# Optimization experiments

Hardware: AMD Instinct MI355X
Metric: run time of the kernel (lower is better)

## Reference

```python
import jax, jax.numpy as jnp
import numpy as np

N = 50000      # nodes
E = 800000     # edges (avg degree 16)
D = 128        # node_dim
H = 3          # total_hops
NE = 16        # num edge types
LN_EPS = 1e-3  # keras LayerNormalization default


def setup_inputs() -> dict:
    key = jax.random.key(0)
    ks = jax.random.split(key, 8)
    scale = 1.0 / np.sqrt(D)
    return {
        "x": jax.random.normal(ks[0], (N, D), jnp.float32),
        "src": jax.random.randint(ks[1], (E,), 0, N, jnp.int32),
        "dest": jax.random.randint(ks[2], (E,), 0, N, jnp.int32),
        "classes": jax.random.randint(ks[3], (E,), 0, NE, jnp.int32),
        "W_src": jax.random.normal(ks[4], (H, D, D), jnp.float32) * scale,
        "b_src": jnp.zeros((H, D), jnp.float32),
        "W_dest": jax.random.normal(ks[5], (H, D, D), jnp.float32) * scale,
        "b_dest": jnp.zeros((H, D), jnp.float32),
        "edge_emb": jax.random.normal(ks[6], (H, NE, D), jnp.float32) * 0.02,
        "ln_gamma": jnp.ones((H, D), jnp.float32),
        "ln_beta": jnp.zeros((H, D), jnp.float32),
    }


def _hop(x, src, dest, classes, Ws, bs, Wd, bd, ee, g, b):
    # dense transforms on nodes [N,D], then gather to edges [E,D]
    s = x @ Ws + bs
    t = x @ Wd + bd
    msgs = jax.nn.relu(s[src] + t[dest] + ee[classes])  # [E,D]
    # unsorted_segment_mean: zero for empty segments (TF semantics)
    summ = jax.ops.segment_sum(msgs, dest, num_segments=N)                    # [N,D]
    cnt = jax.ops.segment_sum(jnp.ones((E, 1), x.dtype), dest, num_segments=N)
    mean = jnp.where(cnt > 0, summ / jnp.maximum(cnt, 1.0), 0.0)
    y = mean + x  # residual add
    mu = jnp.mean(y, axis=-1, keepdims=True)
    var = jnp.mean(jnp.square(y - mu), axis=-1, keepdims=True)
    return g * (y - mu) * jax.lax.rsqrt(var + LN_EPS) + b


def reference(x, src, dest, classes, W_src, b_src, W_dest, b_dest, edge_emb, ln_gamma, ln_beta):
    for i in range(H):
        x = _hop(x, src, dest, classes, W_src[i], b_src[i], W_dest[i], b_dest[i],
                 edge_emb[i], ln_gamma[i], ln_beta[i])
    return x
```

## Files before the change

### kernel.cpp

```cpp
#include <hip/hip_runtime.h>

#define D 128
#define NE 16
#define HOPS 3
#define CAP 96
#define CPAD 32

typedef __attribute__((ext_vector_type(8))) __bf16 bf16x8;
typedef __attribute__((ext_vector_type(4))) __bf16 bf16x4;
typedef __attribute__((ext_vector_type(4))) float f32x4;

#define PK_MASK 0x07FFFFFFu
#define PK_SHIFT 27

__global__ __launch_bounds__(256) void prep_kernel(
    const int* __restrict__ src, const int* __restrict__ dest,
    const int* __restrict__ classes, int* __restrict__ cnt,
    unsigned int* __restrict__ s_pk, int E, int FB,
    const float* __restrict__ Wsrc, const float* __restrict__ Wdst,
    __bf16* __restrict__ WTs, __bf16* __restrict__ WTd, int WB,
    const float* __restrict__ x, __bf16* __restrict__ xb, int n4, int CB) {
  int b = blockIdx.x;
  int tid = threadIdx.x;
  if (b < FB) {
    int e = b * 256 + tid;
    if (e < E) {
      int d = dest[e];
      int p = atomicAdd(&cnt[(size_t)d * CPAD], 1);
      if (p < CAP)
        s_pk[(size_t)d * CAP + p] = (unsigned int)src[e] | ((unsigned int)classes[e] << PK_SHIFT);
    }
  } else if (b < FB + WB) {
    int gid = (b - FB) * 256 + tid;
    int h = gid >> 14;
    int rem = gid & 16383;
    int k = rem >> 7, nn = rem & 127;
    size_t o = (size_t)h * 16384 + nn * 128 + k;
    WTs[o] = (__bf16)Wsrc[gid];
    WTd[o] = (__bf16)Wdst[gid];
  } else {
    int i = (b - FB - WB) * 256 + tid;
    if (i < n4) {
      f32x4 v = ((const f32x4*)x)[i];
      bf16x4 o;
      o[0] = (__bf16)v[0]; o[1] = (__bf16)v[1]; o[2] = (__bf16)v[2]; o[3] = (__bf16)v[3];
      ((bf16x4*)xb)[i] = o;
    }
  }
}

__global__ __launch_bounds__(256) void gemm_dual(const __bf16* __restrict__ xb,
    const __bf16* __restrict__ WTs, const __bf16* __restrict__ WTd,
    const float* __restrict__ bs, const float* __restrict__ bd,
    __bf16* __restrict__ s_b, __bf16* __restrict__ t_b, int n) {
  int w = threadIdx.x >> 6, l = threadIdx.x & 63;
  int l16 = l & 15, q = l >> 4;
  bf16x8 a[2][4];
  #pragma unroll
  for (int rt = 0; rt < 2; ++rt) {
    int rowA = blockIdx.x * 128 + (w + rt * 4) * 16 + l16;
    int rsafe = rowA < n ? rowA : 0;
    #pragma unroll
    for (int ks = 0; ks < 4; ++ks)
      a[rt][ks] = *(const bf16x8*)&xb[(size_t)rsafe * D + ks * 32 + q * 8];
  }
  f32x4 accS[2][8], accT[2][8];
  #pragma unroll
  for (int rt = 0; rt < 2; ++rt)
    #pragma unroll
    for (int n0 = 0; n0 < 8; ++n0) {
      accS[rt][n0] = (f32x4)0.f;
      accT[rt][n0] = (f32x4)0.f;
    }
  #pragma unroll
  for (int n0 = 0; n0 < 8; ++n0) {
    const __bf16* ps = &WTs[(size_t)(n0 * 16 + l16) * D + q * 8];
    const __bf16* pt = &WTd[(size_t)(n0 * 16 + l16) * D + q * 8];
    #pragma unroll
    for (int ks = 0; ks < 4; ++ks) {
      bf16x8 bfs = *(const bf16x8*)(ps + ks * 32);
      bf16x8 bft = *(const bf16x8*)(pt + ks * 32);
      #pragma unroll
      for (int rt = 0; rt < 2; ++rt) {
        accS[rt][n0] = __builtin_amdgcn_mfma_f32_16x16x32_bf16(a[rt][ks], bfs, accS[rt][n0], 0, 0, 0);
        accT[rt][n0] = __builtin_amdgcn_mfma_f32_16x16x32_bf16(a[rt][ks], bft, accT[rt][n0], 0, 0, 0);
      }
    }
  }
  #pragma unroll
  for (int rt = 0; rt < 2; ++rt) {
    int rowD = blockIdx.x * 128 + (w + rt * 4) * 16 + q * 4;
    #pragma unroll
    for (int n0 = 0; n0 < 8; ++n0) {
      int col = n0 * 16 + l16;
      float bS = bs[col], bT = bd[col];
      #pragma unroll
      for (int r = 0; r < 4; ++r) {
        int row = rowD + r;
        if (row < n) {
          s_b[(size_t)row * D + col] = (__bf16)(accS[rt][n0][r] + bS);
          t_b[(size_t)row * D + col] = (__bf16)(accT[rt][n0][r] + bT);
        }
      }
    }
  }
}

__global__ __launch_bounds__(256) void aggregate_kernel(
    const __bf16* __restrict__ s_b, const __bf16* __restrict__ t_b,
    const float* __restrict__ xin,
    const int* __restrict__ cnt_arr,
    const unsigned int* __restrict__ s_pk,
    const float* __restrict__ ee, const float* __restrict__ gamma,
    const float* __restrict__ beta, float* __restrict__ xout,
    __bf16* __restrict__ xb_out, int write_xb, int n) {
  __shared__ float ee_s[NE * D];
  for (int i = threadIdx.x; i < NE * D; i += 256) ee_s[i] = ee[i];
  __syncthreads();
  int wave = threadIdx.x >> 6;
  int lane = threadIdx.x & 63;
  int node = blockIdx.x * 4 + wave;
  if (node >= n) return;
  int quarter = lane >> 4;
  int l16 = lane & 15;
  int d0 = l16 * 8;
  size_t nbase = (size_t)node * D;
  bf16x8 tvb = *(const bf16x8*)&t_b[nbase + d0];
  float tv[8];
  #pragma unroll
  for (int j = 0; j < 8; ++j) tv[j] = (float)tvb[j];
  f32x4 xlo = *(const f32x4*)&xin[nbase + d0];
  f32x4 xhi = *(const f32x4*)&xin[nbase + d0 + 4];
  int cn = cnt_arr[(size_t)node * CPAD];
  if (cn > CAP) cn = CAP;
  int beg = node * CAP;
  int end = beg + cn;
  float acc[8] = {0.f, 0.f, 0.f, 0.f, 0.f, 0.f, 0.f, 0.f};
  int e = beg + quarter;
  for (; e + 4 < end; e += 8) {
    unsigned int v0 = s_pk[e];
    unsigned int v1 = s_pk[e + 4];
    bf16x8 sv0 = *(const bf16x8*)&s_b[(size_t)(v0 & PK_MASK) * D + d0];
    bf16x8 sv1 = *(const bf16x8*)&s_b[(size_t)(v1 & PK_MASK) * D + d0];
    const float* ep0 = &ee_s[(v0 >> PK_SHIFT) * D + d0];
    const float* ep1 = &ee_s[(v1 >> PK_SHIFT) * D + d0];
    f32x4 e0a = *(const f32x4*)ep0, e0b = *(const f32x4*)(ep0 + 4);
    f32x4 e1a = *(const f32x4*)ep1, e1b = *(const f32x4*)(ep1 + 4);
    #pragma unroll
    for (int j = 0; j < 8; ++j) {
      float u0 = (float)sv0[j] + tv[j] + (j < 4 ? e0a[j] : e0b[j - 4]);
      float u1 = (float)sv1[j] + tv[j] + (j < 4 ? e1a[j] : e1b[j - 4]);
      acc[j] += fmaxf(u0, 0.f) + fmaxf(u1, 0.f);
    }
  }
  if (e < end) {
    unsigned int v0 = s_pk[e];
    bf16x8 sv0 = *(const bf16x8*)&s_b[(size_t)(v0 & PK_MASK) * D + d0];
    const float* ep0 = &ee_s[(v0 >> PK_SHIFT) * D + d0];
    f32x4 e0a = *(const f32x4*)ep0, e0b = *(const f32x4*)(ep0 + 4);
    #pragma unroll
    for (int j = 0; j < 8; ++j) {
      float u0 = (float)sv0[j] + tv[j] + (j < 4 ? e0a[j] : e0b[j - 4]);
      acc[j] += fmaxf(u0, 0.f);
    }
  }
  #pragma unroll
  for (int j = 0; j < 8; ++j) {
    acc[j] += __shfl_xor(acc[j], 32);
    acc[j] += __shfl_xor(acc[j], 16);
  }
  float invc = cn > 0 ? 1.f / (float)cn : 0.f;
  float y[8];
  #pragma unroll
  for (int j = 0; j < 8; ++j)
    y[j] = acc[j] * invc + (j < 4 ? xlo[j] : xhi[j - 4]);
  float ssum = 0.f;
  #pragma unroll
  for (int j = 0; j < 8; ++j) ssum += y[j];
  #pragma unroll
  for (int off = 8; off > 0; off >>= 1) ssum += __shfl_xor(ssum, off);
  float mu = ssum * (1.f / (float)D);
  float dv[8], vs = 0.f;
  #pragma unroll
  for (int j = 0; j < 8; ++j) { dv[j] = y[j] - mu; vs += dv[j] * dv[j]; }
  #pragma unroll
  for (int off = 8; off > 0; off >>= 1) vs += __shfl_xor(vs, off);
  float inv = rsqrtf(vs * (1.f / (float)D) + 1e-3f);
  if (quarter == 0) {
    f32x4 g0 = *(const f32x4*)&gamma[d0];
    f32x4 g1 = *(const f32x4*)&gamma[d0 + 4];
    f32x4 b0 = *(const f32x4*)&beta[d0];
    f32x4 b1 = *(const f32x4*)&beta[d0 + 4];
    float o[8];
    #pragma unroll
    for (int j = 0; j < 8; ++j)
      o[j] = (j < 4 ? g0[j] : g1[j - 4]) * dv[j] * inv + (j < 4 ? b0[j] : b1[j - 4]);
    f32x4 o0, o1;
    #pragma unroll
    for (int j = 0; j < 4; ++j) { o0[j] = o[j]; o1[j] = o[j + 4]; }
    *(f32x4*)&xout[nbase + d0] = o0;
    *(f32x4*)&xout[nbase + d0 + 4] = o1;
    if (write_xb) {
      bf16x8 ob;
      #pragma unroll
      for (int j = 0; j < 8; ++j) ob[j] = (__bf16)o[j];
      *(bf16x8*)&xb_out[nbase + d0] = ob;
    }
  }
}

extern "C" void kernel_launch(void* const* d_in, const int* in_sizes, int n_in,
                              void* d_out, int out_size, void* d_ws, size_t ws_size,
                              hipStream_t stream) {
  const float* x0     = (const float*)d_in[0];
  const int*   src    = (const int*)d_in[1];
  const int*   dest   = (const int*)d_in[2];
  const int*   cls    = (const int*)d_in[3];
  const float* W_src  = (const float*)d_in[4];
  const float* b_src  = (const float*)d_in[5];
  const float* W_dest = (const float*)d_in[6];
  const float* b_dest = (const float*)d_in[7];
  const float* ee     = (const float*)d_in[8];
  const float* ln_g   = (const float*)d_in[9];
  const float* ln_b   = (const float*)d_in[10];
  float* out = (float*)d_out;

  const int N = in_sizes[0] / D;
  const int E = in_sizes[1];

  char* p = (char*)d_ws;
  __bf16* s_b = (__bf16*)p;   p += (size_t)N * D * sizeof(__bf16);
  __bf16* t_b = (__bf16*)p;   p += (size_t)N * D * sizeof(__bf16);
  __bf16* xb  = (__bf16*)p;   p += (size_t)N * D * sizeof(__bf16);
  __bf16* WTs = (__bf16*)p;   p += (size_t)HOPS * D * D * sizeof(__bf16);
  __bf16* WTd = (__bf16*)p;   p += (size_t)HOPS * D * D * sizeof(__bf16);
  int* cntb   = (int*)p;      p += (size_t)N * CPAD * sizeof(int);
  unsigned int* s_pk = (unsigned int*)p; p += (size_t)N * CAP * sizeof(unsigned int);

  hipMemsetAsync(cntb, 0, (size_t)N * CPAD * sizeof(int), stream);

  const int FB = (E + 255) / 256;
  const int WB = (HOPS * D * D) / 256;
  const int n4 = N * D / 4;
  const int CB = (n4 + 255) / 256;
  prep_kernel<<<FB + WB + CB, 256, 0, stream>>>(
      src, dest, cls, cntb, s_pk, E, FB,
      W_src, W_dest, WTs, WTd, WB,
      x0, xb, n4, CB);

  const float* xin = x0;
  for (int h = 0; h < HOPS; ++h) {
    gemm_dual<<<(N + 127) / 128, 256, 0, stream>>>(
        xb, WTs + (size_t)h * D * D, WTd + (size_t)h * D * D,
        b_src + (size_t)h * D, b_dest + (size_t)h * D, s_b, t_b, N);
    aggregate_kernel<<<(N + 3) / 4, 256, 0, stream>>>(
        s_b, t_b, xin, cntb, s_pk,
        ee + (size_t)h * NE * D, ln_g + (size_t)h * D, ln_b + (size_t)h * D,
        out, xb, (h < HOPS - 1) ? 1 : 0, N);
    xin = out;
  }
}
```

Measured before the change: 291.5 us.

## Split per-node edge buckets into four sub-buckets with separate atomic counters

The bucketing step now spreads each node's incoming edges over four sub-buckets, one counter per sub-bucket placed on its own cache-line offset, chosen by edge index. This is meant to cut atomic contention on the per-node counter. The aggregation kernel gives each wave quarter its own sub-bucket and unrolls the gather loop four deep to keep more loads in flight. Load balance across quarters now depends on the edge distribution, and each sub-bucket caps at 24 entries, so a node whose edges crowd one sub-bucket can drop edges that the old 96-entry single bucket would have kept.

New measurement: 337.4 us. 15.8% more time.

```diff
diff --git a/kernel.cpp b/kernel.cpp
--- a/kernel.cpp
+++ b/kernel.cpp
@@ -3,7 +3,9 @@
 #define D 128
 #define NE 16
 #define HOPS 3
-#define CAP 96
+#define NSUB 4
+#define SCAP 24
+#define CAP (NSUB * SCAP)
 #define CPAD 32
 
 typedef __attribute__((ext_vector_type(8))) __bf16 bf16x8;
@@ -26,9 +28,11 @@
     int e = b * 256 + tid;
     if (e < E) {
       int d = dest[e];
-      int p = atomicAdd(&cnt[(size_t)d * CPAD], 1);
-      if (p < CAP)
-        s_pk[(size_t)d * CAP + p] = (unsigned int)src[e] | ((unsigned int)classes[e] << PK_SHIFT);
+      int sub = e & (NSUB - 1);
+      int p = atomicAdd(&cnt[(size_t)d * CPAD + sub * 8], 1);
+      if (p < SCAP)
+        s_pk[(size_t)d * CAP + sub * SCAP + p] =
+            (unsigned int)src[e] | ((unsigned int)classes[e] << PK_SHIFT);
     }
   } else if (b < FB + WB) {
     int gid = (b - FB) * 256 + tid;
@@ -131,45 +135,59 @@
   for (int j = 0; j < 8; ++j) tv[j] = (float)tvb[j];
   f32x4 xlo = *(const f32x4*)&xin[nbase + d0];
   f32x4 xhi = *(const f32x4*)&xin[nbase + d0 + 4];
-  int cn = cnt_arr[(size_t)node * CPAD];
-  if (cn > CAP) cn = CAP;
-  int beg = node * CAP;
-  int end = beg + cn;
+
+  int cq = cnt_arr[(size_t)node * CPAD + quarter * 8];
+  if (cq > SCAP) cq = SCAP;
+  int base = node * CAP + quarter * SCAP;
   float acc[8] = {0.f, 0.f, 0.f, 0.f, 0.f, 0.f, 0.f, 0.f};
-  int e = beg + quarter;
-  for (; e + 4 < end; e += 8) {
-    unsigned int v0 = s_pk[e];
-    unsigned int v1 = s_pk[e + 4];
-    bf16x8 sv0 = *(const bf16x8*)&s_b[(size_t)(v0 & PK_MASK) * D + d0];
-    bf16x8 sv1 = *(const bf16x8*)&s_b[(size_t)(v1 & PK_MASK) * D + d0];
-    const float* ep0 = &ee_s[(v0 >> PK_SHIFT) * D + d0];
-    const float* ep1 = &ee_s[(v1 >> PK_SHIFT) * D + d0];
-    f32x4 e0a = *(const f32x4*)ep0, e0b = *(const f32x4*)(ep0 + 4);
-    f32x4 e1a = *(const f32x4*)ep1, e1b = *(const f32x4*)(ep1 + 4);
-    #pragma unroll
-    for (int j = 0; j < 8; ++j) {
-      float u0 = (float)sv0[j] + tv[j] + (j < 4 ? e0a[j] : e0b[j - 4]);
-      float u1 = (float)sv1[j] + tv[j] + (j < 4 ? e1a[j] : e1b[j - 4]);
-      acc[j] += fmaxf(u0, 0.f) + fmaxf(u1, 0.f);
-    }
-  }
-  if (e < end) {
-    unsigned int v0 = s_pk[e];
-    bf16x8 sv0 = *(const bf16x8*)&s_b[(size_t)(v0 & PK_MASK) * D + d0];
-    const float* ep0 = &ee_s[(v0 >> PK_SHIFT) * D + d0];
-    f32x4 e0a = *(const f32x4*)ep0, e0b = *(const f32x4*)(ep0 + 4);
-    #pragma unroll
-    for (int j = 0; j < 8; ++j) {
-      float u0 = (float)sv0[j] + tv[j] + (j < 4 ? e0a[j] : e0b[j - 4]);
-      acc[j] += fmaxf(u0, 0.f);
-    }
-  }
+
+#define EDGE_ACC(V, SV)                                                        \
+  {                                                                            \
+    const float* ep = &ee_s[((V) >> PK_SHIFT) * D + d0];                       \
+    f32x4 ea = *(const f32x4*)ep, eb = *(const f32x4*)(ep + 4);                \
+    _Pragma("unroll")                                                          \
+    for (int j = 0; j < 8; ++j) {                                              \
+      float u = (float)(SV)[j] + tv[j] + (j < 4 ? ea[j] : eb[j - 4]);          \
+      acc[j] += fmaxf(u, 0.f);                                                 \
+    }                                                                          \
+  }
+
+  int i = 0;
+  for (; i + 3 < cq; i += 4) {
+    unsigned int v0 = s_pk[base + i];
+    unsigned int v1 = s_pk[base + i + 1];
+    unsigned int v2 = s_pk[base + i + 2];
+    unsigned int v3 = s_pk[base + i + 3];
+    bf16x8 s0 = *(const bf16x8*)&s_b[(size_t)(v0 & PK_MASK) * D + d0];
+    bf16x8 s1 = *(const bf16x8*)&s_b[(size_t)(v1 & PK_MASK) * D + d0];
+    bf16x8 s2 = *(const bf16x8*)&s_b[(size_t)(v2 & PK_MASK) * D + d0];
+    bf16x8 s3 = *(const bf16x8*)&s_b[(size_t)(v3 & PK_MASK) * D + d0];
+    EDGE_ACC(v0, s0); EDGE_ACC(v1, s1); EDGE_ACC(v2, s2); EDGE_ACC(v3, s3);
+  }
+  if (i + 1 < cq) {
+    unsigned int v0 = s_pk[base + i];
+    unsigned int v1 = s_pk[base + i + 1];
+    bf16x8 s0 = *(const bf16x8*)&s_b[(size_t)(v0 & PK_MASK) * D + d0];
+    bf16x8 s1 = *(const bf16x8*)&s_b[(size_t)(v1 & PK_MASK) * D + d0];
+    EDGE_ACC(v0, s0); EDGE_ACC(v1, s1);
+    i += 2;
+  }
+  if (i < cq) {
+    unsigned int v0 = s_pk[base + i];
+    bf16x8 s0 = *(const bf16x8*)&s_b[(size_t)(v0 & PK_MASK) * D + d0];
+    EDGE_ACC(v0, s0);
+  }
+#undef EDGE_ACC
+
+  int tot = cq;
+  tot += __shfl_xor(tot, 32);
+  tot += __shfl_xor(tot, 16);
   #pragma unroll
   for (int j = 0; j < 8; ++j) {
     acc[j] += __shfl_xor(acc[j], 32);
     acc[j] += __shfl_xor(acc[j], 16);
   }
-  float invc = cn > 0 ? 1.f / (float)cn : 0.f;
+  float invc = tot > 0 ? 1.f / (float)tot : 0.f;
   float y[8];
   #pragma unroll
   for (int j = 0; j < 8; ++j)
```
